# Kernel optimization log

Measured on AMD Instinct MI355X. Metric: run time of the kernel, lower is better.

## Reference

```python
import jax, jax.numpy as jnp
import numpy as np

B, N, S = 8, 8192, 1024
K = 16          # max_degree
HIDDEN = 192    # hidden_dim, divisible by 2*ndim -> no padding in sincos embed
NDIM = 3
MAX_WAVELENGTH = 10000.0


def sincos_embed(coords, dim, ndim):
    # Continuous sin/cos embedding: dim//ndim channels per coordinate,
    # half sin / half cos, geometric frequencies (UPT-style).
    dpw = dim // ndim                          # dims per coordinate (even)
    ar = jnp.arange(0, dpw, 2, dtype=coords.dtype)
    omega = 1.0 / (MAX_WAVELENGTH ** (ar / dpw))   # (dpw/2,)
    out = coords[..., None] * omega            # (..., ndim, dpw/2)
    emb = jnp.concatenate([jnp.sin(out), jnp.cos(out)], axis=-1)  # (..., ndim, dpw)
    return emb.reshape(*coords.shape[:-1], dim)


def knn_gather(x, sidx, k):
    # x: (B,N,ndim), sidx: (B,S) -> (B,S,k,ndim) coords of k nearest neighbors.
    # Equivalent to the original dense NxN dists[sidx] + argsort[:, :k],
    # but only computes the S rows that are used and uses top_k.
    def per_sample(sx, si):
        sp = sx[si]                                            # (S, ndim)
        d = jnp.sum((sp[:, None, :] - sx[None, :, :]) ** 2, -1)  # (S, N)
        _, nbr = jax.lax.top_k(-d, k)                          # k smallest dists
        return sx[nbr]                                         # (S, k, ndim)
    return jax.vmap(per_sample)(x, sidx)


def setup_inputs() -> dict:
    key = jax.random.key(0)
    ks = jax.random.split(key, 6)
    scale = 0.02
    return {
        "input_points": jax.random.normal(ks[0], (B, N, NDIM), dtype=jnp.float32),
        "supernode_idxs": jax.random.randint(ks[1], (B, S), 0, N),
        "w_in": jax.random.normal(ks[2], (NDIM, HIDDEN), dtype=jnp.float32) * scale,
        "b_in": jnp.zeros((HIDDEN,), dtype=jnp.float32),
        "w1": jax.random.normal(ks[3], (HIDDEN, HIDDEN), dtype=jnp.float32) * scale,
        "b1": jnp.zeros((HIDDEN,), dtype=jnp.float32),
        "w2": jax.random.normal(ks[4], (HIDDEN, HIDDEN), dtype=jnp.float32) * scale,
        "b2": jnp.zeros((HIDDEN,), dtype=jnp.float32),
    }


def reference(input_points, supernode_idxs, w_in, b_in, w1, b1, w2, b2):
    nbr = knn_gather(input_points, supernode_idxs, K)      # (B,S,K,3)
    # input projection + continuous sincos positional embedding
    h = nbr @ w_in + b_in + sincos_embed(nbr, HIDDEN, NDIM)  # (B,S,K,H)
    # message net: Dense -> gelu -> Dense
    h = jax.nn.gelu(h @ w1 + b1)
    h = h @ w2 + b2
    # mean-pool over neighbors per supernode
    return jnp.mean(h, axis=-2)                            # (B,S,H)
```

## Files before the change

kernel.cpp:

```cpp
#include <hip/hip_runtime.h>
#include <stdint.h>

#define NB   8
#define NPTS 8192
#define NS   1024
#define NK   16
#define NH   192
#define KP1  224
#define HROW 236
#define QTR  2048
#define MR   64

typedef float    f32x4 __attribute__((ext_vector_type(4)));
typedef short    s16x8 __attribute__((ext_vector_type(8)));
typedef uint32_t u32;
typedef unsigned long long u64;

constexpr float OMEGA[32] = {
  1.0f, 0.74989420933245585f, 0.56234132519034907f, 0.42169650342858223f,
  0.31622776601683794f, 0.23713737056616552f, 0.17782794100389229f, 0.13335214321633237f,
  0.1f, 0.074989420933245585f, 0.056234132519034907f, 0.042169650342858223f,
  0.031622776601683794f, 0.023713737056616552f, 0.017782794100389229f, 0.013335214321633237f,
  0.01f, 0.0074989420933245585f, 0.0056234132519034907f, 0.0042169650342858223f,
  0.0031622776601683794f, 0.0023713737056616552f, 0.0017782794100389229f, 0.0013335214321633237f,
  0.001f, 0.00074989420933245585f, 0.00056234132519034907f, 0.00042169650342858223f,
  0.00031622776601683794f, 0.00023713737056616552f, 0.00017782794100389229f, 0.00013335214321633237f };

__device__ __forceinline__ uint16_t f2bf(float f) {
  u32 u = __float_as_uint(f);
  return (uint16_t)((u + 0x7FFFu + ((u >> 16) & 1u)) >> 16);
}
__device__ __forceinline__ u32 pk2bf(float f0, float f1) {
  return ((__float_as_uint(f0) + 0x8000u) >> 16) |
         ((__float_as_uint(f1) + 0x8000u) & 0xFFFF0000u);
}

__global__ void __launch_bounds__(64) prep_weights(
    const float* __restrict__ w_in, const float* __restrict__ b_in,
    const float* __restrict__ w1, const float* __restrict__ b1,
    const float* __restrict__ w2,
    uint16_t* __restrict__ wT1e, uint16_t* __restrict__ wT2) {
  const int n = blockIdx.x, t = threadIdx.x;
  float p0 = 0, p1 = 0, p2 = 0, pb = 0;
  #pragma unroll
  for (int kk = 0; kk < 3; ++kk) {
    int c = kk * 64 + t;
    float w1cn = w1[c * NH + n];
    wT1e[n * KP1 + c] = f2bf(w1cn);
    wT2 [n * NH  + c] = f2bf(w2[c * NH + n]);
    p0 = fmaf(w_in[0 * NH + c], w1cn, p0);
    p1 = fmaf(w_in[1 * NH + c], w1cn, p1);
    p2 = fmaf(w_in[2 * NH + c], w1cn, p2);
    pb = fmaf(b_in[c], w1cn, pb);
  }
  #pragma unroll
  for (int off = 32; off; off >>= 1) {
    p0 += __shfl_down(p0, off);
    p1 += __shfl_down(p1, off);
    p2 += __shfl_down(p2, off);
    pb += __shfl_down(pb, off);
  }
  if (t == 0) {
    wT1e[n * KP1 + 192] = f2bf(p0);
    wT1e[n * KP1 + 193] = f2bf(p1);
    wT1e[n * KP1 + 194] = f2bf(p2);
    wT1e[n * KP1 + 195] = f2bf(pb + b1[n]);
  }
  if (t >= 4 && t < 32) wT1e[n * KP1 + 192 + t] = 0;
}

__global__ void __launch_bounds__(512, 8) knn_kernel(const float* __restrict__ pts,
                                                     const int* __restrict__ sidx,
                                                     u64* __restrict__ keys) {
  __shared__ float2 XY[QTR];
  __shared__ float  Zs[QTR];
  const int bid = blockIdx.x;
  const int b = bid >> 7;
  const int chunk = (bid >> 2) & 31;
  const int quarter = bid & 3;
  const int pbase = quarter * QTR;
  const float* pb = pts + ((size_t)b * NPTS + pbase) * 3;
  for (int i = threadIdx.x; i < QTR; i += 512) {
    XY[i] = float2{pb[3 * i], pb[3 * i + 1]};
    Zs[i] = pb[3 * i + 2];
  }
  __syncthreads();
  const int wave = threadIdx.x >> 6, lane = threadIdx.x & 63;
  const int sbase = chunk * 32 + wave * 4;

  float sx[4], sy[4], sz[4], minD[4], Td[4];
  u32 minI[4];
  u64 arr[4], T[4];
  #pragma unroll
  for (int q = 0; q < 4; ++q) {
    int si = sidx[b * NS + sbase + q];
    const float* qp = pts + ((size_t)b * NPTS + si) * 3;
    sx[q] = qp[0]; sy[q] = qp[1]; sz[q] = qp[2];
    minD[q] = __uint_as_float(0x7F800000u);
    minI[q] = 0xFFFFFFFFu;
  }

  for (int t = 0; t < QTR / 64; ++t) {
    int lj = t * 64 + lane;
    float2 xy = XY[lj];
    float z = Zs[lj];
    #pragma unroll
    for (int q = 0; q < 4; ++q) {
      float dx = xy.x - sx[q], dy = xy.y - sy[q], dz = z - sz[q];
      float d = __fadd_rn(__fadd_rn(__fmul_rn(dx, dx), __fmul_rn(dy, dy)),
                          __fmul_rn(dz, dz));
      bool c = d < minD[q];
      minD[q] = c ? d : minD[q];
      minI[q] = c ? (u32)(pbase + lj) : minI[q];
    }
  }

  #pragma unroll
  for (int q = 0; q < 4; ++q) {
    u64 key = ((u64)__float_as_uint(minD[q]) << 32) | minI[q];
    #pragma unroll
    for (int k = 2; k <= 64; k <<= 1) {
      #pragma unroll
      for (int jj = k >> 1; jj > 0; jj >>= 1) {
        u64 p = __shfl_xor(key, jj);
        bool takeMin = (((lane & jj) == 0) == ((lane & k) == 0));
        key = (takeMin == (p < key)) ? p : key;
      }
    }
    arr[q] = (lane < 16) ? key : ~0ull;
    T[q] = __shfl(key, 15);
    Td[q] = __uint_as_float((u32)(T[q] >> 32));
  }

  for (int t = 0; t < QTR / 64; ++t) {
    int lj = t * 64 + lane;
    float2 xy = XY[lj];
    float z = Zs[lj];
    #pragma unroll
    for (int q = 0; q < 4; ++q) {
      float dx = xy.x - sx[q], dy = xy.y - sy[q], dz = z - sz[q];
      float d = __fadd_rn(__fadd_rn(__fmul_rn(dx, dx), __fmul_rn(dy, dy)),
                          __fmul_rn(dz, dz));
      u64 ball = __ballot(d <= Td[q] && (u32)(pbase + lj) != minI[q]);
      if (ball) {
        u64 key = ((u64)__float_as_uint(d) << 32) | (u32)(pbase + lj);
        do {
          int src = __builtin_ctzll(ball);
          ball &= ball - 1;
          u64 k2 = __shfl(key, src);
          if (k2 < T[q]) {
            int r = __popcll(__ballot(arr[q] < k2));
            u64 up = __shfl_up(arr[q], 1);
            if (lane == r) arr[q] = k2;
            else if (lane > r && lane < 16) arr[q] = up;
            T[q] = __shfl(arr[q], 15);
            Td[q] = __uint_as_float((u32)(T[q] >> 32));
          }
        } while (ball);
      }
    }
  }
  #pragma unroll
  for (int q = 0; q < 4; ++q)
    if (lane < 16)
      keys[((size_t)(b * NS + sbase + q)) * 64 + quarter * 16 + lane] = arr[q];
}

__device__ __forceinline__ float h0ch(int c, float c0, float c1, float c2) {
  if (c >= 196) return 0.0f;
  if (c == 195) return 1.0f;
  if (c == 192) return c0;
  if (c == 193) return c1;
  if (c == 194) return c2;
  int dd = c >> 6, i = c & 63, m = i & 31;
  float coord = (dd == 0) ? c0 : ((dd == 1) ? c1 : c2);
  float arg = coord * OMEGA[m];
  return (i < 32) ? __sinf(arg) : __cosf(arg);
}

__device__ __forceinline__ float gelu_f(float x) {
  float v = -1.5957691216057308f * __fmaf_rn(0.044715f * x, x * x, x);
  return x * __builtin_amdgcn_rcpf(1.0f + __expf(v));
}

__global__ void __launch_bounds__(256) mlp_kernel(
    const float* __restrict__ pts, const u64* __restrict__ keys,
    const float* __restrict__ b2v,
    const uint16_t* __restrict__ wT1e, const uint16_t* __restrict__ wT2,
    float* __restrict__ out) {
  __shared__ uint16_t hbuf[MR * HROW];
  __shared__ int nbrL[MR];
  const int g = blockIdx.x, tid = threadIdx.x;
  const int wave = tid >> 6, lane = tid & 63;
  const int lrow = lane & 15, lg = lane >> 4;

  {
    int list = lane >> 4, pos = lane & 15;
    int rpos = (list & 1) ? (15 - pos) : pos;
    u64 key = keys[((size_t)g * 4 + wave) * 64 + list * 16 + rpos];
    #pragma unroll
    for (int jj = 16; jj > 0; jj >>= 1) {
      u64 p = __shfl_xor(key, jj);
      bool takeMin = (((lane & jj) == 0) == ((lane & 32) == 0));
      key = (takeMin == (p < key)) ? p : key;
    }
    #pragma unroll
    for (int jj = 32; jj > 0; jj >>= 1) {
      u64 p = __shfl_xor(key, jj);
      bool takeMin = ((lane & jj) == 0);
      key = (takeMin == (p < key)) ? p : key;
    }
    if (lane < 16) nbrL[wave * 16 + lane] = (int)(u32)key;
  }
  __syncthreads();

  {
    int r = tid >> 2, qt = tid & 3;
    int grow = g * MR + r;
    int b = grow >> 14;
    int pidx = nbrL[r];
    const float* pp = pts + ((size_t)b * NPTS + pidx) * 3;
    float c0 = pp[0], c1 = pp[1], c2 = pp[2];
    uint16_t* hrow = hbuf + r * HROW;
    if (qt == 0) {
      #pragma unroll
      for (int jj = 0; jj < 14; ++jj) {
        const int c = jj * 4;
        uint2 pk;
        pk.x = pk2bf(h0ch(c,     c0, c1, c2), h0ch(c + 1, c0, c1, c2));
        pk.y = pk2bf(h0ch(c + 2, c0, c1, c2), h0ch(c + 3, c0, c1, c2));
        *(uint2*)(hrow + c) = pk;
      }
    } else if (qt == 1) {
      #pragma unroll
      for (int jj = 0; jj < 14; ++jj) {
        const int c = 56 + jj * 4;
        uint2 pk;
        pk.x = pk2bf(h0ch(c,     c0, c1, c2), h0ch(c + 1, c0, c1, c2));
        pk.y = pk2bf(h0ch(c + 2, c0, c1, c2), h0ch(c + 3, c0, c1, c2));
        *(uint2*)(hrow + c) = pk;
      }
    } else if (qt == 2) {
      #pragma unroll
      for (int jj = 0; jj < 14; ++jj) {
        const int c = 112 + jj * 4;
        uint2 pk;
        pk.x = pk2bf(h0ch(c,     c0, c1, c2), h0ch(c + 1, c0, c1, c2));
        pk.y = pk2bf(h0ch(c + 2, c0, c1, c2), h0ch(c + 3, c0, c1, c2));
        *(uint2*)(hrow + c) = pk;
      }
    } else {
      #pragma unroll
      for (int jj = 0; jj < 14; ++jj) {
        const int c = 168 + jj * 4;
        uint2 pk;
        pk.x = pk2bf(h0ch(c,     c0, c1, c2), h0ch(c + 1, c0, c1, c2));
        pk.y = pk2bf(h0ch(c + 2, c0, c1, c2), h0ch(c + 3, c0, c1, c2));
        *(uint2*)(hrow + c) = pk;
      }
    }
  }
  __syncthreads();

  f32x4 acc1[3][4] = {};
  {
    const uint16_t* wbase = wT1e + (size_t)(wave * 48 + lrow) * KP1 + lg * 8;
    uint4 anx[3];
    #pragma unroll
    for (int nt = 0; nt < 3; ++nt) anx[nt] = *(const uint4*)(wbase + nt * 16 * KP1);
    #pragma unroll
    for (int kk = 0; kk < 7; ++kk) {
      uint4 acur[3];
      #pragma unroll
      for (int nt = 0; nt < 3; ++nt) acur[nt] = anx[nt];
      if (kk < 6) {
        #pragma unroll
        for (int nt = 0; nt < 3; ++nt)
          anx[nt] = *(const uint4*)(wbase + nt * 16 * KP1 + (kk + 1) * 32);
      }
      s16x8 bm[4];
      #pragma unroll
      for (int mt = 0; mt < 4; ++mt)
        bm[mt] = __builtin_bit_cast(s16x8,
                   *(const uint4*)(hbuf + (mt * 16 + lrow) * HROW + kk * 32 + lg * 8));
      #pragma unroll
      for (int nt = 0; nt < 3; ++nt)
        #pragma unroll
        for (int mt = 0; mt < 4; ++mt)
          acc1[nt][mt] = __builtin_amdgcn_mfma_f32_16x16x32_bf16(
              __builtin_bit_cast(s16x8, acur[nt]), bm[mt], acc1[nt][mt], 0, 0, 0);
    }
  }
  __syncthreads();

  {
    #pragma unroll
    for (int nt = 0; nt < 3; ++nt) {
      #pragma unroll
      for (int mt = 0; mt < 4; ++mt) {
        uint2 pk;
        pk.x = pk2bf(gelu_f(acc1[nt][mt][0]), gelu_f(acc1[nt][mt][1]));
        pk.y = pk2bf(gelu_f(acc1[nt][mt][2]), gelu_f(acc1[nt][mt][3]));
        *(uint2*)(hbuf + (mt * 16 + lrow) * HROW + wave * 48 + nt * 16 + lg * 4) = pk;
      }
    }
  }
  __syncthreads();

  f32x4 acc2[4][3] = {};
  {
    const uint16_t* w2base = wT2 + (size_t)(wave * 48 + lrow) * NH + lg * 8;
    uint4 bnx[3];
    #pragma unroll
    for (int nt = 0; nt < 3; ++nt) bnx[nt] = *(const uint4*)(w2base + nt * 16 * NH);
    #pragma unroll
    for (int kk = 0; kk < 6; ++kk) {
      uint4 bcur[3];
      #pragma unroll
      for (int nt = 0; nt < 3; ++nt) bcur[nt] = bnx[nt];
      if (kk < 5) {
        #pragma unroll
        for (int nt = 0; nt < 3; ++nt)
          bnx[nt] = *(const uint4*)(w2base + nt * 16 * NH + (kk + 1) * 32);
      }
      s16x8 am[4];
      #pragma unroll
      for (int mt = 0; mt < 4; ++mt)
        am[mt] = __builtin_bit_cast(s16x8,
                   *(const uint4*)(hbuf + (mt * 16 + lrow) * HROW + kk * 32 + lg * 8));
      #pragma unroll
      for (int mt = 0; mt < 4; ++mt)
        #pragma unroll
        for (int nt = 0; nt < 3; ++nt)
          acc2[mt][nt] = __builtin_amdgcn_mfma_f32_16x16x32_bf16(
              am[mt], __builtin_bit_cast(s16x8, bcur[nt]), acc2[mt][nt], 0, 0, 0);
    }
  }

  {
    #pragma unroll
    for (int mt = 0; mt < 4; ++mt) {
      #pragma unroll
      for (int nt = 0; nt < 3; ++nt) {
        float ssum = acc2[mt][nt][0] + acc2[mt][nt][1] + acc2[mt][nt][2] + acc2[mt][nt][3];
        ssum += __shfl_xor(ssum, 16);
        ssum += __shfl_xor(ssum, 32);
        if (lane < 16) {
          int col = wave * 48 + nt * 16 + lrow;
          out[(size_t)(g * 4 + mt) * NH + col] = ssum * 0.0625f + b2v[col];
        }
      }
    }
  }
}

extern "C" void kernel_launch(void* const* d_in, const int* in_sizes, int n_in,
                              void* d_out, int out_size, void* d_ws, size_t ws_size,
                              hipStream_t stream) {
  (void)in_sizes; (void)n_in; (void)out_size; (void)ws_size;
  const float* pts  = (const float*)d_in[0];
  const int*   sidx = (const int*)d_in[1];
  const float* w_in = (const float*)d_in[2];
  const float* b_in = (const float*)d_in[3];
  const float* w1   = (const float*)d_in[4];
  const float* b1   = (const float*)d_in[5];
  const float* w2   = (const float*)d_in[6];
  const float* b2   = (const float*)d_in[7];
  float* out = (float*)d_out;

  u64* keys = (u64*)d_ws;
  uint16_t* wT1e = (uint16_t*)((char*)d_ws + (size_t)NB * NS * 64 * 8);
  uint16_t* wT2  = wT1e + NH * KP1;

  hipLaunchKernelGGL(prep_weights, dim3(NH), dim3(64), 0, stream,
                     w_in, b_in, w1, b1, w2, wT1e, wT2);

  hipLaunchKernelGGL(knn_kernel, dim3(NB * 128), dim3(512), 0, stream,
                     pts, sidx, keys);

  hipLaunchKernelGGL(mlp_kernel, dim3(NB * NS / 4), dim3(256), 0, stream,
                     pts, keys, b2, wT1e, wT2, out);
}
```

Measured before the change: 100.8 us.

## Pack KNN distance math into float2 pairs and double MLP block rows

The KNN kernel now stores X, Y and Z in separate shared arrays and processes two candidate points per lane with float2 vector arithmetic. This aims to use packed FP32 ops and halve loop iterations, at the cost of splitting the threshold-insert loop into two ballot passes. The MLP kernel now runs 512 threads on 8 supernodes (128 rows) per block, so each weight fragment is reused across two row halves. This adds shared memory and register pressure, and it changes the launch bounds of both kernels.

```diff
diff --git a/kernel.cpp b/kernel.cpp
--- a/kernel.cpp
+++ b/kernel.cpp
@@ -9,8 +9,9 @@
 #define KP1  224
 #define HROW 236
 #define QTR  2048
-#define MR   64
-
+#define MR   128
+
+typedef float    f32x2 __attribute__((ext_vector_type(2)));
 typedef float    f32x4 __attribute__((ext_vector_type(4)));
 typedef short    s16x8 __attribute__((ext_vector_type(8)));
 typedef uint32_t u32;
@@ -69,11 +70,13 @@
   if (t >= 4 && t < 32) wT1e[n * KP1 + 192 + t] = 0;
 }
 
-__global__ void __launch_bounds__(512, 8) knn_kernel(const float* __restrict__ pts,
+__global__ void __launch_bounds__(512, 4) knn_kernel(const float* __restrict__ pts,
                                                      const int* __restrict__ sidx,
                                                      u64* __restrict__ keys) {
-  __shared__ float2 XY[QTR];
-  __shared__ float  Zs[QTR];
+  #pragma clang fp contract(off)
+  __shared__ f32x2 Xp[QTR / 2];
+  __shared__ f32x2 Yp[QTR / 2];
+  __shared__ f32x2 Zp[QTR / 2];
   const int bid = blockIdx.x;
   const int b = bid >> 7;
   const int chunk = (bid >> 2) & 31;
@@ -81,43 +84,53 @@
   const int pbase = quarter * QTR;
   const float* pb = pts + ((size_t)b * NPTS + pbase) * 3;
   for (int i = threadIdx.x; i < QTR; i += 512) {
-    XY[i] = float2{pb[3 * i], pb[3 * i + 1]};
-    Zs[i] = pb[3 * i + 2];
+    ((float*)Xp)[i] = pb[3 * i + 0];
+    ((float*)Yp)[i] = pb[3 * i + 1];
+    ((float*)Zp)[i] = pb[3 * i + 2];
   }
   __syncthreads();
   const int wave = threadIdx.x >> 6, lane = threadIdx.x & 63;
   const int sbase = chunk * 32 + wave * 4;
 
-  float sx[4], sy[4], sz[4], minD[4], Td[4];
-  u32 minI[4];
+  f32x2 sx2[4], sy2[4], sz2[4];
+  float mnDx[4], mnDy[4], Td[4];
+  u32 mnI0[4], mnI1[4], minI[4];
   u64 arr[4], T[4];
   #pragma unroll
   for (int q = 0; q < 4; ++q) {
     int si = sidx[b * NS + sbase + q];
     const float* qp = pts + ((size_t)b * NPTS + si) * 3;
-    sx[q] = qp[0]; sy[q] = qp[1]; sz[q] = qp[2];
-    minD[q] = __uint_as_float(0x7F800000u);
-    minI[q] = 0xFFFFFFFFu;
-  }
-
-  for (int t = 0; t < QTR / 64; ++t) {
-    int lj = t * 64 + lane;
-    float2 xy = XY[lj];
-    float z = Zs[lj];
+    sx2[q] = f32x2{qp[0], qp[0]};
+    sy2[q] = f32x2{qp[1], qp[1]};
+    sz2[q] = f32x2{qp[2], qp[2]};
+    mnDx[q] = __uint_as_float(0x7F800000u);
+    mnDy[q] = __uint_as_float(0x7F800000u);
+    mnI0[q] = 0xFFFFFFFFu; mnI1[q] = 0xFFFFFFFFu;
+  }
+
+  for (int t = 0; t < QTR / 128; ++t) {
+    int lp = t * 64 + lane;
+    f32x2 xs = Xp[lp], ys = Yp[lp], zs = Zp[lp];
+    u32 j0 = (u32)(pbase + 2 * lp);
     #pragma unroll
     for (int q = 0; q < 4; ++q) {
-      float dx = xy.x - sx[q], dy = xy.y - sy[q], dz = z - sz[q];
-      float d = __fadd_rn(__fadd_rn(__fmul_rn(dx, dx), __fmul_rn(dy, dy)),
-                          __fmul_rn(dz, dz));
-      bool c = d < minD[q];
-      minD[q] = c ? d : minD[q];
-      minI[q] = c ? (u32)(pbase + lj) : minI[q];
+      f32x2 dx = xs - sx2[q], dy = ys - sy2[q], dz = zs - sz2[q];
+      f32x2 d = ((dx * dx) + (dy * dy)) + (dz * dz);
+      bool c0 = d.x < mnDx[q];
+      mnDx[q] = c0 ? d.x : mnDx[q];
+      mnI0[q] = c0 ? j0 : mnI0[q];
+      bool c1 = d.y < mnDy[q];
+      mnDy[q] = c1 ? d.y : mnDy[q];
+      mnI1[q] = c1 ? (j0 + 1) : mnI1[q];
     }
   }
 
   #pragma unroll
   for (int q = 0; q < 4; ++q) {
-    u64 key = ((u64)__float_as_uint(minD[q]) << 32) | minI[q];
+    u64 k0 = ((u64)__float_as_uint(mnDx[q]) << 32) | mnI0[q];
+    u64 k1 = ((u64)__float_as_uint(mnDy[q]) << 32) | mnI1[q];
+    u64 key = (k0 < k1) ? k0 : k1;
+    minI[q] = (u32)key;
     #pragma unroll
     for (int k = 2; k <= 64; k <<= 1) {
       #pragma unroll
@@ -132,22 +145,24 @@
     Td[q] = __uint_as_float((u32)(T[q] >> 32));
   }
 
-  for (int t = 0; t < QTR / 64; ++t) {
-    int lj = t * 64 + lane;
-    float2 xy = XY[lj];
-    float z = Zs[lj];
+  for (int t = 0; t < QTR / 128; ++t) {
+    int lp = t * 64 + lane;
+    f32x2 xs = Xp[lp], ys = Yp[lp], zs = Zp[lp];
+    u32 j0 = (u32)(pbase + 2 * lp);
     #pragma unroll
     for (int q = 0; q < 4; ++q) {
-      float dx = xy.x - sx[q], dy = xy.y - sy[q], dz = z - sz[q];
-      float d = __fadd_rn(__fadd_rn(__fmul_rn(dx, dx), __fmul_rn(dy, dy)),
-                          __fmul_rn(dz, dz));
-      u64 ball = __ballot(d <= Td[q] && (u32)(pbase + lj) != minI[q]);
-      if (ball) {
-        u64 key = ((u64)__float_as_uint(d) << 32) | (u32)(pbase + lj);
-        do {
-          int src = __builtin_ctzll(ball);
-          ball &= ball - 1;
-          u64 k2 = __shfl(key, src);
+      f32x2 dx = xs - sx2[q], dy = ys - sy2[q], dz = zs - sz2[q];
+      f32x2 d = ((dx * dx) + (dy * dy)) + (dz * dz);
+      bool c0 = (d.x <= Td[q]) && (j0 != minI[q]);
+      bool c1 = (d.y <= Td[q]) && ((j0 + 1) != minI[q]);
+      u64 gate = __ballot(c0 || c1);
+      if (gate) {
+        u64 b0 = __ballot(c0);
+        u64 key0 = ((u64)__float_as_uint(d.x) << 32) | j0;
+        while (b0) {
+          int src = __builtin_ctzll(b0);
+          b0 &= b0 - 1;
+          u64 k2 = __shfl(key0, src);
           if (k2 < T[q]) {
             int r = __popcll(__ballot(arr[q] < k2));
             u64 up = __shfl_up(arr[q], 1);
@@ -156,7 +171,22 @@
             T[q] = __shfl(arr[q], 15);
             Td[q] = __uint_as_float((u32)(T[q] >> 32));
           }
-        } while (ball);
+        }
+        u64 b1 = __ballot(c1);
+        u64 key1 = ((u64)__float_as_uint(d.y) << 32) | (j0 + 1);
+        while (b1) {
+          int src = __builtin_ctzll(b1);
+          b1 &= b1 - 1;
+          u64 k2 = __shfl(key1, src);
+          if (k2 < T[q]) {
+            int r = __popcll(__ballot(arr[q] < k2));
+            u64 up = __shfl_up(arr[q], 1);
+            if (lane == r) arr[q] = k2;
+            else if (lane > r && lane < 16) arr[q] = up;
+            T[q] = __shfl(arr[q], 15);
+            Td[q] = __uint_as_float((u32)(T[q] >> 32));
+          }
+        }
       }
     }
   }
@@ -183,7 +213,7 @@
   return x * __builtin_amdgcn_rcpf(1.0f + __expf(v));
 }
 
-__global__ void __launch_bounds__(256) mlp_kernel(
+__global__ void __launch_bounds__(512, 4) mlp_kernel(
     const float* __restrict__ pts, const u64* __restrict__ keys,
     const float* __restrict__ b2v,
     const uint16_t* __restrict__ wT1e, const uint16_t* __restrict__ wT2,
@@ -193,11 +223,13 @@
   const int g = blockIdx.x, tid = threadIdx.x;
   const int wave = tid >> 6, lane = tid & 63;
   const int lrow = lane & 15, lg = lane >> 4;
+  const int mh = wave >> 2;
+  const int ns = wave & 3;
 
   {
     int list = lane >> 4, pos = lane & 15;
     int rpos = (list & 1) ? (15 - pos) : pos;
-    u64 key = keys[((size_t)g * 4 + wave) * 64 + list * 16 + rpos];
+    u64 key = keys[((size_t)g * 8 + wave) * 64 + list * 16 + rpos];
     #pragma unroll
     for (int jj = 16; jj > 0; jj >>= 1) {
       u64 p = __shfl_xor(key, jj);
@@ -264,7 +296,7 @@
 
   f32x4 acc1[3][4] = {};
   {
-    const uint16_t* wbase = wT1e + (size_t)(wave * 48 + lrow) * KP1 + lg * 8;
+    const uint16_t* wbase = wT1e + (size_t)(ns * 48 + lrow) * KP1 + lg * 8;
     uint4 anx[3];
     #pragma unroll
     for (int nt = 0; nt < 3; ++nt) anx[nt] = *(const uint4*)(wbase + nt * 16 * KP1);
@@ -282,7 +314,7 @@
       #pragma unroll
       for (int mt = 0; mt < 4; ++mt)
         bm[mt] = __builtin_bit_cast(s16x8,
-                   *(const uint4*)(hbuf + (mt * 16 + lrow) * HROW + kk * 32 + lg * 8));
+                   *(const uint4*)(hbuf + (mh * 64 + mt * 16 + lrow) * HROW + kk * 32 + lg * 8));
       #pragma unroll
       for (int nt = 0; nt < 3; ++nt)
         #pragma unroll
@@ -301,7 +333,7 @@
         uint2 pk;
         pk.x = pk2bf(gelu_f(acc1[nt][mt][0]), gelu_f(acc1[nt][mt][1]));
         pk.y = pk2bf(gelu_f(acc1[nt][mt][2]), gelu_f(acc1[nt][mt][3]));
-        *(uint2*)(hbuf + (mt * 16 + lrow) * HROW + wave * 48 + nt * 16 + lg * 4) = pk;
+        *(uint2*)(hbuf + (mh * 64 + mt * 16 + lrow) * HROW + ns * 48 + nt * 16 + lg * 4) = pk;
       }
     }
   }
@@ -309,7 +341,7 @@
 
   f32x4 acc2[4][3] = {};
   {
-    const uint16_t* w2base = wT2 + (size_t)(wave * 48 + lrow) * NH + lg * 8;
+    const uint16_t* w2base = wT2 + (size_t)(ns * 48 + lrow) * NH + lg * 8;
     uint4 bnx[3];
     #pragma unroll
     for (int nt = 0; nt < 3; ++nt) bnx[nt] = *(const uint4*)(w2base + nt * 16 * NH);
@@ -327,7 +359,7 @@
       #pragma unroll
       for (int mt = 0; mt < 4; ++mt)
         am[mt] = __builtin_bit_cast(s16x8,
-                   *(const uint4*)(hbuf + (mt * 16 + lrow) * HROW + kk * 32 + lg * 8));
+                   *(const uint4*)(hbuf + (mh * 64 + mt * 16 + lrow) * HROW + kk * 32 + lg * 8));
       #pragma unroll
       for (int mt = 0; mt < 4; ++mt)
         #pragma unroll
@@ -346,8 +378,8 @@
         ssum += __shfl_xor(ssum, 16);
         ssum += __shfl_xor(ssum, 32);
         if (lane < 16) {
-          int col = wave * 48 + nt * 16 + lrow;
-          out[(size_t)(g * 4 + mt) * NH + col] = ssum * 0.0625f + b2v[col];
+          int col = ns * 48 + nt * 16 + lrow;
+          out[(size_t)(g * 8 + mh * 4 + mt) * NH + col] = ssum * 0.0625f + b2v[col];
         }
       }
     }
@@ -378,6 +410,6 @@
   hipLaunchKernelGGL(knn_kernel, dim3(NB * 128), dim3(512), 0, stream,
                      pts, sidx, keys);
 
-  hipLaunchKernelGGL(mlp_kernel, dim3(NB * NS / 4), dim3(256), 0, stream,
+  hipLaunchKernelGGL(mlp_kernel, dim3(NB * NS / 8), dim3(512), 0, stream,
                      pts, keys, b2, wT1e, wT2, out);
 }
```

Measured after the change: 100.7 us. Within noise of the previous version (-0.1%).
